# Kernel optimization log

Hardware: AMD Instinct MI355X
Metric: run time of the kernel (lower is better)

## Reference

```python
import jax, jax.numpy as jnp
import numpy as np
from jax import lax

N_NODES = 10000
N_EDGES = 320000


def setup_inputs() -> dict:
    key = jax.random.key(0)
    ks = jax.random.split(key, 7)
    B, H, N, F = 4, 24, N_NODES, 32
    hid = 64
    x = jax.random.normal(ks[0], (B, H, N, F), dtype=jnp.float32)
    mask = jax.random.uniform(ks[1], (B, H), dtype=jnp.float32)
    edge_index = jax.random.randint(ks[2], (2, N_EDGES), 0, N, dtype=jnp.int32)
    W1 = jax.random.normal(ks[3], (F + 1, hid), dtype=jnp.float32) * (1.0 / np.sqrt(F + 1))
    b1 = jax.random.normal(ks[4], (hid,), dtype=jnp.float32) * 0.02
    W2 = jax.random.normal(ks[5], (hid, F), dtype=jnp.float32) * (1.0 / np.sqrt(hid))
    b2 = jax.random.normal(ks[6], (F,), dtype=jnp.float32) * 0.02
    return {"x": x, "mask": mask, "edge_index": edge_index,
            "W1": W1, "b1": b1, "W2": W2, "b2": b2}


def _gcn_norm(edge_index, num_nodes):
    # PyG GCNConv default: add self loops, symmetric normalization.
    loops = jnp.arange(num_nodes, dtype=edge_index.dtype)
    src = jnp.concatenate([edge_index[0], loops])
    dst = jnp.concatenate([edge_index[1], loops])
    deg = jax.ops.segment_sum(jnp.ones_like(dst, dtype=jnp.float32), dst,
                              num_segments=num_nodes)
    dinv = jnp.where(deg > 0, lax.rsqrt(jnp.maximum(deg, 1e-12)), 0.0)
    norm = dinv[src] * dinv[dst]  # [E']
    return src, dst, norm


def reference(x, mask, edge_index, W1, b1, W2, b2):
    B, H, N, F = x.shape
    src, dst, norm = _gcn_norm(edge_index, N)

    def gcn(h, W, b):
        # h: [B, N, Fin] -> lin, then normalized neighbor aggregation, then bias
        hw = h @ W                                   # [B, N, Fout]
        msg = hw[:, src, :].transpose(1, 0, 2)       # [E', B, Fout]
        msg = msg * norm[:, None, None]
        agg = jax.ops.segment_sum(msg, dst, num_segments=N)  # [N, B, Fout]
        return agg.transpose(1, 0, 2) + b

    def per_hour(carry, inp):
        xh, mh = inp                                 # xh: [B, N, F], mh: [B]
        mc = jnp.broadcast_to(mh[:, None, None], (B, N, 1))
        h = jnp.concatenate([xh, mc], axis=-1)       # [B, N, F+1]
        out = jnp.tanh(gcn(gcn(h, W1, b1), W2, b2))  # [B, N, F]
        return carry, out

    _, outs = lax.scan(per_hour, None,
                       (x.transpose(1, 0, 2, 3), mask.T))  # [H, B, N, F]
    return outs.transpose(1, 0, 2, 3)                     # [B, H, N, F]
```

## Files before the change

### kernel.cpp

```cpp
#include <hip/hip_runtime.h>
#include <hip/hip_fp16.h>

#define NN 10000
#define FF 32
#define PG 4
#define NGRP 24

typedef __attribute__((ext_vector_type(2))) float f32x2;

__device__ __forceinline__ unsigned short f2h(float f){
  union { unsigned short s; _Float16 h; } c; c.h = (_Float16)f; return c.s;
}

__device__ __forceinline__ void fmix2p(float& ax, float& ay, unsigned wpk, unsigned h){
  asm("v_fma_mix_f32 %0, %2, %3, %0 op_sel_hi:[1,1,0]\n\t"
      "v_fma_mix_f32 %1, %2, %3, %1 op_sel:[0,1,0] op_sel_hi:[1,1,0]"
      : "+v"(ax), "+v"(ay) : "s"(wpk), "v"(h));
}
__device__ __forceinline__ void fmix2s(float& ax, float& ay, float w, unsigned h){
  asm("v_fma_mix_f32 %0, %2, %3, %0 op_sel_hi:[0,1,0]\n\t"
      "v_fma_mix_f32 %1, %2, %3, %1 op_sel:[0,1,0] op_sel_hi:[0,1,0]"
      : "+v"(ax), "+v"(ay) : "s"(w), "v"(h));
}

__device__ __forceinline__ void pkfma(f32x2& acc, f32x2 w, f32x2 x){
  asm("v_pk_fma_f32 %0, %1, %2, %0" : "+v"(acc) : "s"(w), "v"(x));
}

__global__ void k_count(const int* __restrict__ dst, int* __restrict__ cnt,
                        unsigned* __restrict__ csr, int csrcap, int E){
  int e = blockIdx.x * 256 + threadIdx.x;
  if (e >= E) return;
  csr[e] = 0u;
  int e2 = e + E;
  if (e2 < csrcap) csr[e2] = 0u;
  atomicAdd(&cnt[dst[e]], 1);
}

__global__ __launch_bounds__(256) void k_prep(const int* __restrict__ cnt,
    int2* __restrict__ oe, float* __restrict__ dinv, int* __restrict__ gtop,
    const float* __restrict__ W1, const float* __restrict__ W2,
    const float* __restrict__ b1, float* __restrict__ W12, float* __restrict__ bb){
  int bx = blockIdx.x, tid = threadIdx.x;
  if (bx < 40){
    int i = bx * 256 + tid;
    if (i < NN){
      int c = cnt[i];
      int pad = (c + 3) & ~3;
      int start = atomicAdd(gtop, pad);
      oe[i] = make_int2(start, start + pad);
      dinv[i] = rsqrtf((float)(c + 1));
    }
  } else {
    int j = (bx - 40) * 256 + tid;
    if (j < 33 * 32){
      int k = j >> 5, c = j & 31;
      float s = 0.f;
      for (int m = 0; m < 64; ++m) s += W1[k * 64 + m] * W2[m * 32 + c];
      W12[j] = s;
    } else if (j < 33 * 32 + 32){
      int c = j - 33 * 32;
      float s = 0.f;
      for (int m = 0; m < 64; ++m) s += b1[m] * W2[m * 32 + c];
      bb[c] = s;
    }
  }
}

__global__ void k_scatter(const int* __restrict__ ei, const int2* __restrict__ oe,
                          int* __restrict__ cur, const float* __restrict__ dinv,
                          unsigned* __restrict__ csr, float* __restrict__ srow, int E){
  int e = blockIdx.x * 256 + threadIdx.x;
  if (e >= E) return;
  int s = ei[e], d = ei[E + e];
  float ds = dinv[s];
  int pos = oe[d].x + atomicAdd(&cur[d], 1);
  csr[pos] = ((unsigned)s << 16) | (unsigned)f2h(ds);
  atomicAdd(&srow[d], ds);
}

__global__ __launch_bounds__(256) void k_gemm1(const float* __restrict__ x,
    const float* __restrict__ mask, const float* __restrict__ W12,
    unsigned* __restrict__ hw){
  const int pg = blockIdx.y;
  const int n  = blockIdx.x * 256 + threadIdx.x;
  const int grp = pg >> 2, p = pg & 3;
  const float mv = mask[pg];
  const f32x2* Wp = (const f32x2*)W12;
  f32x2 acc[16];
  #pragma unroll
  for (int qf = 0; qf < 16; ++qf){
    f32x2 w = Wp[32 * 16 + qf];
    acc[qf].x = mv * w.x; acc[qf].y = mv * w.y;
  }
  if (n >= NN) return;
  const float4* xp = (const float4*)(x + (size_t)pg * (NN * FF) + (size_t)n * FF);
  float xv[32];
  #pragma unroll
  for (int i = 0; i < 8; ++i){
    float4 v = xp[i];
    xv[4*i]   = v.x; xv[4*i+1] = v.y;
    xv[4*i+2] = v.z; xv[4*i+3] = v.w;
  }
  #pragma unroll
  for (int k = 0; k < 32; ++k){
    f32x2 xk2; xk2.x = xv[k]; xk2.y = xv[k];
    #pragma unroll
    for (int qf = 0; qf < 16; ++qf) pkfma(acc[qf], Wp[k * 16 + qf], xk2);
  }
  unsigned* hwg = hw + (size_t)grp * (NN * 64) + ((size_t)n << 6) + (p << 4);
  #pragma unroll
  for (int j = 0; j < 4; ++j){
    uint4 u;
    u.x = (unsigned)f2h(acc[4*j+0].x) | ((unsigned)f2h(acc[4*j+0].y) << 16);
    u.y = (unsigned)f2h(acc[4*j+1].x) | ((unsigned)f2h(acc[4*j+1].y) << 16);
    u.z = (unsigned)f2h(acc[4*j+2].x) | ((unsigned)f2h(acc[4*j+2].y) << 16);
    u.w = (unsigned)f2h(acc[4*j+3].x) | ((unsigned)f2h(acc[4*j+3].y) << 16);
    ((uint4*)hwg)[j] = u;
  }
}

__device__ __forceinline__ void map_block(int bx, int& grp, int& chunk){
  int r  = bx / 5000;
  int w8 = bx % 5000;
  grp   = r * 8 + (w8 & 7);
  chunk = w8 >> 3;
}

#define ROWB(w) ((((unsigned)(w)) >> 8) & 0xFFFF00u)
__device__ __forceinline__ void agg_edges(int e0, int e1,
    const unsigned* __restrict__ csr, const char* __restrict__ Vb, int loff,
    float& ax, float& ay){
  int nq = (e1 - e0) >> 2;
  if (nq <= 0) return;
  const int4* c4 = (const int4*)(csr + e0);
  const int qlast = nq - 1;
  #define VLD(w) (*(const unsigned*)(Vb + (unsigned)(ROWB(w) + loff)))
  int4 cA, cB, cC, cD;
  int4 cA2, cB2, cC2, cD2;
  int4 cA3, cB3, cC3, cD3;
  unsigned rA0,rA1,rA2,rA3, rB0,rB1,rB2,rB3;
  unsigned rC0,rC1,rC2,rC3, rD0,rD1,rD2,rD3;
  {
    int i1 = 1<=qlast?1:qlast, i2 = 2<=qlast?2:qlast, i3 = 3<=qlast?3:qlast;
    cA = c4[0]; cB = c4[i1]; cC = c4[i2]; cD = c4[i3];
    int i4 = 4<=qlast?4:qlast, i5 = 5<=qlast?5:qlast;
    int i6 = 6<=qlast?6:qlast, i7 = 7<=qlast?7:qlast;
    cA2 = c4[i4]; cB2 = c4[i5]; cC2 = c4[i6]; cD2 = c4[i7];
    int i8 = 8<=qlast?8:qlast, i9 = 9<=qlast?9:qlast;
    int i10 = 10<=qlast?10:qlast, i11 = 11<=qlast?11:qlast;
    cA3 = c4[i8]; cB3 = c4[i9]; cC3 = c4[i10]; cD3 = c4[i11];
    rA0 = VLD(cA.x); rA1 = VLD(cA.y); rA2 = VLD(cA.z); rA3 = VLD(cA.w);
    rB0 = VLD(cB.x); rB1 = VLD(cB.y); rB2 = VLD(cB.z); rB3 = VLD(cB.w);
    rC0 = VLD(cC.x); rC1 = VLD(cC.y); rC2 = VLD(cC.z); rC3 = VLD(cC.w);
    rD0 = VLD(cD.x); rD1 = VLD(cD.y); rD2 = VLD(cD.z); rD3 = VLD(cD.w);
  }
  int q = 0;
  #define AGG_STEP(cX, cX2, cX3, r0, r1, r2, r3)                        \
    do {                                                                \
      fmix2p(ax, ay, (unsigned)cX.x, r0);                               \
      fmix2p(ax, ay, (unsigned)cX.y, r1);                               \
      fmix2p(ax, ay, (unsigned)cX.z, r2);                               \
      fmix2p(ax, ay, (unsigned)cX.w, r3);                               \
      r0 = VLD(cX2.x); r1 = VLD(cX2.y);                                 \
      r2 = VLD(cX2.z); r3 = VLD(cX2.w);                                 \
      cX = cX2; cX2 = cX3;                                              \
    } while (0)
  for (; q + 3 < nq; q += 4){
    AGG_STEP(cA, cA2, cA3, rA0,rA1,rA2,rA3);
    AGG_STEP(cB, cB2, cB3, rB0,rB1,rB2,rB3);
    AGG_STEP(cC, cC2, cC3, rC0,rC1,rC2,rC3);
    AGG_STEP(cD, cD2, cD3, rD0,rD1,rD2,rD3);
    int j0 = q+12 <= qlast ? q+12 : qlast;
    int j1 = q+13 <= qlast ? q+13 : qlast;
    int j2 = q+14 <= qlast ? q+14 : qlast;
    int j3 = q+15 <= qlast ? q+15 : qlast;
    cA3 = c4[j0]; cB3 = c4[j1]; cC3 = c4[j2]; cD3 = c4[j3];
  }
  #undef AGG_STEP
  #undef VLD
  int rem = nq - q;
  if (rem > 0){
    fmix2p(ax, ay, (unsigned)cA.x, rA0);
    fmix2p(ax, ay, (unsigned)cA.y, rA1);
    fmix2p(ax, ay, (unsigned)cA.z, rA2);
    fmix2p(ax, ay, (unsigned)cA.w, rA3);
  }
  if (rem > 1){
    fmix2p(ax, ay, (unsigned)cB.x, rB0);
    fmix2p(ax, ay, (unsigned)cB.y, rB1);
    fmix2p(ax, ay, (unsigned)cB.z, rB2);
    fmix2p(ax, ay, (unsigned)cB.w, rB3);
  }
  if (rem > 2){
    fmix2p(ax, ay, (unsigned)cC.x, rC0);
    fmix2p(ax, ay, (unsigned)cC.y, rC1);
    fmix2p(ax, ay, (unsigned)cC.z, rC2);
    fmix2p(ax, ay, (unsigned)cC.w, rC3);
  }
}

__global__ __launch_bounds__(256) void k_agg1(const int2* __restrict__ oe,
    const unsigned* __restrict__ csr, const float* __restrict__ dinv,
    const unsigned int* __restrict__ V, unsigned int* __restrict__ T){
  int grp, chunk; map_block(blockIdx.x, grp, chunk);
  int tid = threadIdx.x;
  int l = tid & 63;
  int wv = __builtin_amdgcn_readfirstlane(tid) >> 6;
  const char* Vb = (const char*)(V + (size_t)grp * (NN * 64));
  unsigned int* Tg = T + (size_t)grp * (NN * 64);
  int loff = l * 4;
  for (int it = 0; it < 4; ++it){
    int n = chunk * 16 + wv * 4 + it;
    float din = dinv[n];
    int2 ee = oe[n];
    unsigned sv = *(const unsigned*)(Vb + (unsigned)((n << 8) + loff));
    float ax = 0.f, ay = 0.f;
    fmix2s(ax, ay, din, sv);
    agg_edges(ee.x, ee.y, csr, Vb, loff, ax, ay);
    Tg[((size_t)n << 6) + l] =
        (unsigned)f2h(din * ax) | ((unsigned)f2h(din * ay) << 16);
  }
}

__global__ __launch_bounds__(256) void k_agg2(const int2* __restrict__ oe,
    const unsigned* __restrict__ csr, const float* __restrict__ dinv,
    const float* __restrict__ srow, const float* __restrict__ bb,
    const float* __restrict__ b2, const unsigned int* __restrict__ V,
    float* __restrict__ out){
  int grp, chunk; map_block(blockIdx.x, grp, chunk);
  int tid = threadIdx.x;
  int l = tid & 63;
  int wv = __builtin_amdgcn_readfirstlane(tid) >> 6;
  int p = l >> 4, fi = l & 15;
  const char* Vb = (const char*)(V + (size_t)grp * (NN * 64));
  int pg = grp * PG + p;
  float2 bbq = ((const float2*)bb)[fi];
  float2 b2q = ((const float2*)b2)[fi];
  float* outp = out + (size_t)pg * (NN * FF);
  int loff = l * 4;
  for (int it = 0; it < 4; ++it){
    int n = chunk * 16 + wv * 4 + it;
    float din = dinv[n];
    int2 ee = oe[n];
    unsigned sv = *(const unsigned*)(Vb + (unsigned)((n << 8) + loff));
    float ax = 0.f, ay = 0.f;
    fmix2s(ax, ay, din, sv);
    agg_edges(ee.x, ee.y, csr, Vb, loff, ax, ay);
    float sr = din * (din + srow[n]);
    float2 o;
    o.x = tanhf(din * ax + sr * bbq.x + b2q.x);
    o.y = tanhf(din * ay + sr * bbq.y + b2q.y);
    ((float2*)(outp + (size_t)n * FF))[fi] = o;
  }
}

extern "C" void kernel_launch(void* const* d_in, const int* in_sizes, int n_in,
                              void* d_out, int out_size, void* d_ws, size_t ws_size,
                              hipStream_t stream){
  const float* x    = (const float*)d_in[0];
  const float* mask = (const float*)d_in[1];
  const int*   ei   = (const int*)d_in[2];
  const float* W1   = (const float*)d_in[3];
  const float* b1   = (const float*)d_in[4];
  const float* W2   = (const float*)d_in[5];
  const float* b2   = (const float*)d_in[6];
  float* out = (float*)d_out;
  const int E = in_sizes[2] / 2;
  const int CSRCAP = E + 3 * NN + 64;

  char* wsp = (char*)d_ws;
  auto alloc = [&](size_t bytes) -> char* {
    char* p = wsp; wsp += (bytes + 255) & ~(size_t)255; return p;
  };
  int*   cnt  = (int*)  alloc((size_t)NN * 4);
  int*   cur  = (int*)  alloc((size_t)NN * 4);
  float* srow = (float*)alloc((size_t)NN * 4);
  int*   gtop = (int*)  alloc(256);
  float* dinv = (float*)alloc((size_t)NN * 4);
  int2*  oe   = (int2*) alloc((size_t)NN * 8);
  float* W12  = (float*)alloc(33 * 32 * 4);
  float* bbv  = (float*)alloc(32 * 4);
  unsigned* csr = (unsigned*)alloc((size_t)CSRCAP * 4);
  const size_t per_group = (size_t)NN * 64 * 4;
  unsigned int* hw = (unsigned int*)alloc((size_t)NGRP * per_group);
  unsigned int* t1 = (unsigned int*)alloc((size_t)NGRP * per_group);

  size_t zspan = (size_t)((char*)dinv - (char*)cnt);
  hipMemsetAsync(cnt, 0, zspan, stream);
  k_count  <<<(E + 255) / 256, 256, 0, stream>>>(ei + E, cnt, csr, CSRCAP, E);
  k_prep   <<<45, 256, 0, stream>>>(cnt, oe, dinv, gtop, W1, W2, b1, W12, bbv);
  k_scatter<<<(E + 255) / 256, 256, 0, stream>>>(ei, oe, cur, dinv, csr, srow, E);

  k_gemm1<<<dim3(40, 96), 256, 0, stream>>>(x, mask, W12, hw);
  k_agg1 <<<15000, 256, 0, stream>>>(oe, csr, dinv, hw, t1);
  k_agg2 <<<15000, 256, 0, stream>>>(oe, csr, dinv, srow, bbv, b2, t1, out);
}
```

Measured before the change: 490.5 us.

## Stage x tile through LDS in gemm1 and split aggregation into per-round launches

```diff
diff --git a/kernel.cpp b/kernel.cpp
--- a/kernel.cpp
+++ b/kernel.cpp
@@ -82,8 +82,10 @@
 __global__ __launch_bounds__(256) void k_gemm1(const float* __restrict__ x,
     const float* __restrict__ mask, const float* __restrict__ W12,
     unsigned* __restrict__ hw){
+  __shared__ float xs[32][257];
   const int pg = blockIdx.y;
-  const int n  = blockIdx.x * 256 + threadIdx.x;
+  const int n0 = blockIdx.x * 256;
+  const int t  = threadIdx.x;
   const int grp = pg >> 2, p = pg & 3;
   const float mv = mask[pg];
   const f32x2* Wp = (const f32x2*)W12;
@@ -93,18 +95,23 @@
     f32x2 w = Wp[32 * 16 + qf];
     acc[qf].x = mv * w.x; acc[qf].y = mv * w.y;
   }
-  if (n >= NN) return;
-  const float4* xp = (const float4*)(x + (size_t)pg * (NN * FF) + (size_t)n * FF);
-  float xv[32];
+  const float4* xb = ((const float4*)(x + (size_t)pg * (NN * FF))) + (size_t)n0 * 8;
   #pragma unroll
   for (int i = 0; i < 8; ++i){
-    float4 v = xp[i];
-    xv[4*i]   = v.x; xv[4*i+1] = v.y;
-    xv[4*i+2] = v.z; xv[4*i+3] = v.w;
-  }
+    int L = (i << 8) + t;
+    int r = L >> 3, c4 = (L & 7) << 2;
+    float4 v = make_float4(0.f, 0.f, 0.f, 0.f);
+    if (n0 + r < NN) v = xb[L];
+    xs[c4 + 0][r] = v.x; xs[c4 + 1][r] = v.y;
+    xs[c4 + 2][r] = v.z; xs[c4 + 3][r] = v.w;
+  }
+  __syncthreads();
+  const int n = n0 + t;
+  if (n >= NN) return;
   #pragma unroll
   for (int k = 0; k < 32; ++k){
-    f32x2 xk2; xk2.x = xv[k]; xk2.y = xv[k];
+    float xk = xs[k][t];
+    f32x2 xk2; xk2.x = xk; xk2.y = xk;
     #pragma unroll
     for (int qf = 0; qf < 16; ++qf) pkfma(acc[qf], Wp[k * 16 + qf], xk2);
   }
@@ -118,13 +125,6 @@
     u.w = (unsigned)f2h(acc[4*j+3].x) | ((unsigned)f2h(acc[4*j+3].y) << 16);
     ((uint4*)hwg)[j] = u;
   }
-}
-
-__device__ __forceinline__ void map_block(int bx, int& grp, int& chunk){
-  int r  = bx / 5000;
-  int w8 = bx % 5000;
-  grp   = r * 8 + (w8 & 7);
-  chunk = w8 >> 3;
 }
 
 #define ROWB(w) ((((unsigned)(w)) >> 8) & 0xFFFF00u)
@@ -202,8 +202,8 @@
 
 __global__ __launch_bounds__(256) void k_agg1(const int2* __restrict__ oe,
     const unsigned* __restrict__ csr, const float* __restrict__ dinv,
-    const unsigned int* __restrict__ V, unsigned int* __restrict__ T){
-  int grp, chunk; map_block(blockIdx.x, grp, chunk);
+    const unsigned int* __restrict__ V, unsigned int* __restrict__ T, int r){
+  int grp = r * 8 + (blockIdx.x & 7), chunk = blockIdx.x >> 3;
   int tid = threadIdx.x;
   int l = tid & 63;
   int wv = __builtin_amdgcn_readfirstlane(tid) >> 6;
@@ -227,8 +227,8 @@
     const unsigned* __restrict__ csr, const float* __restrict__ dinv,
     const float* __restrict__ srow, const float* __restrict__ bb,
     const float* __restrict__ b2, const unsigned int* __restrict__ V,
-    float* __restrict__ out){
-  int grp, chunk; map_block(blockIdx.x, grp, chunk);
+    float* __restrict__ out, int r){
+  int grp = r * 8 + (blockIdx.x & 7), chunk = blockIdx.x >> 3;
   int tid = threadIdx.x;
   int l = tid & 63;
   int wv = __builtin_amdgcn_readfirstlane(tid) >> 6;
@@ -293,6 +293,8 @@
   k_scatter<<<(E + 255) / 256, 256, 0, stream>>>(ei, oe, cur, dinv, csr, srow, E);
 
   k_gemm1<<<dim3(40, 96), 256, 0, stream>>>(x, mask, W12, hw);
-  k_agg1 <<<15000, 256, 0, stream>>>(oe, csr, dinv, hw, t1);
-  k_agg2 <<<15000, 256, 0, stream>>>(oe, csr, dinv, srow, bbv, b2, t1, out);
-}
+  for (int r = 0; r < 3; ++r){
+    k_agg1<<<5000, 256, 0, stream>>>(oe, csr, dinv, hw, t1, r);
+    k_agg2<<<5000, 256, 0, stream>>>(oe, csr, dinv, srow, bbv, b2, t1, out, r);
+  }
+}
```

Measured after the change: 515.8 us. +5.2%, slower.
